# Optimization experiments

Hardware: AMD Instinct MI355X
Metric: run time of the kernel (lower is better)

The kernel has to match this reference:

```python
import math
import jax, jax.numpy as jnp
import numpy as np

B, N, C, H = 8, 512, 1024, 16
HD = C // H


def setup_inputs() -> dict:
    key = jax.random.key(0)
    ks = jax.random.split(key, 10)
    s = 0.02
    return {
        "x": jax.random.normal(ks[0], (B, N, C), jnp.float32),
        "mu": jax.random.normal(ks[1], (B, N, C), jnp.float32),
        "logvar": jax.random.normal(ks[2], (B, N, C), jnp.float32) * 0.1,
        "alpha": jax.random.uniform(ks[3], (B, N, 1), jnp.float32, 0.05, 1.0),
        "pi": jax.random.uniform(ks[4], (B, N, 1), jnp.float32, 0.05, 1.0),
        "z": jax.random.normal(ks[5], (B, N, C), jnp.float32),
        "w_q": jax.random.normal(ks[6], (C, C), jnp.float32) * s,
        "w_k": jax.random.normal(ks[7], (C, C), jnp.float32) * s,
        "w_v": jax.random.normal(ks[8], (C, C), jnp.float32) * s,
        "w_p": jax.random.normal(ks[9], (C, C), jnp.float32) * s,
        "b_p": jnp.zeros((C,), jnp.float32),
    }


def reference(x, mu, logvar, alpha, pi, z, w_q, w_k, w_v, w_p, b_p):
    # Non-meta NVIB path (set_mata_training_mode=False, qkv_bias=False).
    sqrt_hd = math.sqrt(HD)
    q = x @ w_q.T                                   # (B,N,C)
    biased_var = jnp.exp(logvar) + sqrt_hd          # (B,Nl,C)
    k = (mu / biased_var) @ w_k.T                   # (B,Nl,C)
    v = (sqrt_hd / biased_var * mu) @ w_v.T         # (B,Nl,C)

    def split_heads(t):
        b, n, _ = t.shape
        return t.reshape(b, n, H, HD).transpose(0, 2, 1, 3)  # (B,H,n,HD)

    qh, kh, vh = split_heads(q), split_heads(k), split_heads(v)
    attn = jnp.einsum("bhnd,bhmd->bhnm", qh, kh)    # (B,H,N,Nl)
    # additive log-alpha minus L2-norm bias, broadcast over heads and queries
    l2 = 0.5 * jnp.sum((mu / jnp.sqrt(biased_var)) ** 2, axis=-1)  # (B,Nl)
    bias = jnp.log(alpha[..., 0]) - l2              # (B,Nl)
    attn = attn + bias[:, None, None, :]
    attn = jax.nn.softmax(attn, axis=-1)
    out = jnp.einsum("bhnm,bhmd->bhnd", attn, vh)   # (B,H,N,HD)
    out = out.transpose(0, 2, 1, 3).reshape(x.shape[0], x.shape[1], C)
    out = out @ w_p.T + b_p
    return (out, attn)
```

## Files before the change

kernel.cpp:

```cpp
#include <hip/hip_runtime.h>
#include <hip/hip_bf16.h>

#define B_  8
#define N_  512
#define C_  1024
#define H_  16
#define HD_ 64
#define M_  4096

typedef float  f32x4  __attribute__((ext_vector_type(4)));
typedef __bf16 bf16x8 __attribute__((ext_vector_type(8)));
typedef unsigned short ushort_t;

__device__ __forceinline__ ushort_t f2bf(float f) {
  union { float f; unsigned int u; } un; un.f = f;
  unsigned int u = un.u;
  return (ushort_t)((u + 0x7fffu + ((u >> 16) & 1u)) >> 16);
}

__device__ __forceinline__ void gload16(const void* g, void* l) {
  __builtin_amdgcn_global_load_lds((const __attribute__((address_space(1))) void*)g,
                                   (__attribute__((address_space(3))) void*)l, 16, 0, 0);
}
#define SBAR()  __builtin_amdgcn_s_barrier()
#define SCHED() __builtin_amdgcn_sched_barrier(0)
#define VMCNT4() asm volatile("s_waitcnt vmcnt(4)" ::: "memory")
#define VMCNT0() asm volatile("s_waitcnt vmcnt(0)" ::: "memory")


__global__ __launch_bounds__(256) void prep_pack_kernel(
    const float* __restrict__ x, const float* __restrict__ mu,
    const float* __restrict__ logvar,
    const float* __restrict__ wq, const float* __restrict__ wk,
    const float* __restrict__ wv, const float* __restrict__ wp,
    ushort_t* __restrict__ xb, ushort_t* __restrict__ kp, ushort_t* __restrict__ vp,
    ushort_t* __restrict__ wb, float* __restrict__ l2part) {
  const int bid = blockIdx.x, t = threadIdx.x;
  const int row = t >> 1, cg = (t & 1) * 16;
  const int c0 = cg >> 3;

  if (bid < 1024) {
    const int mt = bid >> 5, kt = bid & 31;
    const size_t src = (size_t)(mt * 128 + row) * 1024 + kt * 32 + cg;
    ushort_t tx[16] __attribute__((aligned(16)));
    ushort_t tk[16] __attribute__((aligned(16)));
    ushort_t tv[16] __attribute__((aligned(16)));
    float l2 = 0.f;
#pragma unroll
    for (int j = 0; j < 4; ++j) {
      float4 xv = *(const float4*)(x + src + j * 4);
      float4 mv = *(const float4*)(mu + src + j * 4);
      float4 lv = *(const float4*)(logvar + src + j * 4);
      float xa[4] = {xv.x, xv.y, xv.z, xv.w};
      float ma[4] = {mv.x, mv.y, mv.z, mv.w};
      float la[4] = {lv.x, lv.y, lv.z, lv.w};
#pragma unroll
      for (int i = 0; i < 4; ++i) {
        int e = j * 4 + i;
        float bv  = __expf(la[i]) + 8.0f;
        float inv = 1.0f / bv;
        float kf  = ma[i] * inv;
        l2 += ma[i] * kf;
        tx[e] = f2bf(xa[i]); tk[e] = f2bf(kf); tv[e] = f2bf(8.0f * kf);
      }
    }
    const size_t tb = (size_t)((mt * 32 + kt) * 4) * 1024 + row * 8;
    *(bf16x8*)(xb + tb + c0 * 1024)       = *(const bf16x8*)(tx);
    *(bf16x8*)(xb + tb + (c0 + 1) * 1024) = *(const bf16x8*)(tx + 8);
    *(bf16x8*)(kp + tb + c0 * 1024)       = *(const bf16x8*)(tk);
    *(bf16x8*)(kp + tb + (c0 + 1) * 1024) = *(const bf16x8*)(tk + 8);
    *(bf16x8*)(vp + tb + c0 * 1024)       = *(const bf16x8*)(tv);
    *(bf16x8*)(vp + tb + (c0 + 1) * 1024) = *(const bf16x8*)(tv + 8);
    l2 += __shfl_xor(l2, 1);
    if ((t & 1) == 0) l2part[(size_t)(mt * 128 + row) * 32 + kt] = l2;
  } else {
    const int idx = bid - 1024;
    const int sel = idx >> 8, nt = (idx >> 5) & 7, kt = idx & 31;
    const float* src = sel == 0 ? wq : sel == 1 ? wk : sel == 2 ? wv : wp;
    const size_t so = (size_t)(nt * 128 + row) * 1024 + kt * 32 + cg;
    ushort_t tw[16] __attribute__((aligned(16)));
#pragma unroll
    for (int j = 0; j < 4; ++j) {
      float4 v = *(const float4*)(src + so + j * 4);
      tw[j * 4 + 0] = f2bf(v.x); tw[j * 4 + 1] = f2bf(v.y);
      tw[j * 4 + 2] = f2bf(v.z); tw[j * 4 + 3] = f2bf(v.w);
    }
    ushort_t* dst = wb + (size_t)sel * 1048576;
    const size_t tb = (size_t)((nt * 32 + kt) * 4) * 1024 + row * 8;
    *(bf16x8*)(dst + tb + c0 * 1024)       = *(const bf16x8*)(tw);
    *(bf16x8*)(dst + tb + (c0 + 1) * 1024) = *(const bf16x8*)(tw + 8);
  }
}

__device__ __forceinline__ void gemm_tile_r3(const ushort_t* __restrict__ Ag,
                                             const ushort_t* __restrict__ Wg,
                                             int amt, int ant, f32x4 acc[4][4],
                                             ushort_t* lds) {
  const int t = threadIdx.x;
  const int w = t >> 6, lane = t & 63;
  const int wm = w >> 1, wn = w & 1;
  const int chunk = lane >> 4, r15 = lane & 15;
  const int s0 = t, s1 = t + 256;

#define RSTAGE(kt, buf)                                                           \
  do {                                                                            \
    const ushort_t* sa = Ag + (size_t)(amt * 32 + (kt)) * 4096;                   \
    const ushort_t* sb = Wg + (size_t)(ant * 32 + (kt)) * 4096;                   \
    gload16(sa + s0 * 8, lds + (buf) * 4096 + (s0 & ~63) * 8);                    \
    gload16(sa + s1 * 8, lds + (buf) * 4096 + (s1 & ~63) * 8);                    \
    gload16(sb + s0 * 8, lds + 12288 + (buf) * 4096 + (s0 & ~63) * 8);            \
    gload16(sb + s1 * 8, lds + 12288 + (buf) * 4096 + (s1 & ~63) * 8);            \
  } while (0)

#define RCOMPUTE(j)                                                               \
  do {                                                                            \
    const ushort_t* Ab = lds + (j) * 4096;                                        \
    const ushort_t* Bb = lds + 12288 + (j) * 4096;                                \
    bf16x8 af[4], bw[4];                                                          \
    _Pragma("unroll")                                                             \
    for (int mi = 0; mi < 4; ++mi)                                                \
      af[mi] = *(const bf16x8*)(Ab + (chunk * 128 + wm * 64 + mi * 16 + r15) * 8);\
    _Pragma("unroll")                                                             \
    for (int ni = 0; ni < 4; ++ni)                                                \
      bw[ni] = *(const bf16x8*)(Bb + (chunk * 128 + wn * 64 + ni * 16 + r15) * 8);\
    __builtin_amdgcn_s_setprio(1);                                                \
    _Pragma("unroll")                                                             \
    for (int mi = 0; mi < 4; ++mi)                                                \
      _Pragma("unroll")                                                           \
      for (int ni = 0; ni < 4; ++ni)                                              \
        acc[mi][ni] = __builtin_amdgcn_mfma_f32_16x16x32_bf16(af[mi], bw[ni],     \
                                                              acc[mi][ni], 0, 0, 0); \
    __builtin_amdgcn_s_setprio(0);                                                \
    SCHED();                                                                      \
  } while (0)

  RSTAGE(0, 0); RSTAGE(1, 1);
  VMCNT4();
  SBAR(); SCHED();
  for (int kt0 = 0; kt0 < 30; kt0 += 3) {
    RSTAGE(kt0 + 2, 2); RCOMPUTE(0); VMCNT4(); SBAR(); SCHED();
    RSTAGE(kt0 + 3, 0); RCOMPUTE(1); VMCNT4(); SBAR(); SCHED();
    RSTAGE(kt0 + 4, 1); RCOMPUTE(2); VMCNT4(); SBAR(); SCHED();
  }
  RCOMPUTE(0); VMCNT0(); SBAR(); SCHED();
  RCOMPUTE(1);
#undef RSTAGE
#undef RCOMPUTE
}

__global__ __launch_bounds__(256, 3) void gemm_qkv_kernel(
    const ushort_t* __restrict__ xb, const ushort_t* __restrict__ kp,
    const ushort_t* __restrict__ vp, const ushort_t* __restrict__ wb,
    const float* __restrict__ alpha, const float* __restrict__ l2part,
    float* __restrict__ biasv,
    ushort_t* __restrict__ Qhs, ushort_t* __restrict__ Khs, ushort_t* __restrict__ Vts) {
  __shared__ ushort_t lds[24576];
  const int fid = blockIdx.x;
  const int xcd = fid & 7, vl = fid >> 3;
  const int z = vl >> 5, r = vl & 31;
  const int bx = (xcd & 3) * 8 + (r & 7);
  const int by = (xcd >> 2) * 4 + (r >> 3);
  const ushort_t* Ag = z == 0 ? xb : z == 1 ? kp : vp;
  const ushort_t* Wg = wb + (size_t)z * 1048576;
  const int m0 = bx * 128, n0 = by * 128;
  const int t = threadIdx.x;

  if (z == 0 && by == 0 && t < 128) {
    int row = m0 + t;
    const float* p = l2part + (size_t)row * 32;
    float s = 0.f;
#pragma unroll
    for (int j = 0; j < 8; ++j) {
      float4 v = *(const float4*)(p + j * 4);
      s += (v.x + v.y) + (v.z + v.w);
    }
    biasv[row] = __logf(alpha[row]) - 0.5f * s;
  }

  f32x4 acc[4][4] = {};
  gemm_tile_r3(Ag, Wg, bx, by, acc, lds);
  const int w = t >> 6, lane = t & 63;
  const int wm = w >> 1, wn = w & 1;
  const int hi = lane >> 4, r15 = lane & 15;
  const int b = m0 >> 9, h0 = n0 >> 6;

  __syncthreads();
  if (z < 2) {
    ushort_t* T = lds;
#pragma unroll
    for (int mi = 0; mi < 4; ++mi)
#pragma unroll
      for (int ni = 0; ni < 4; ++ni)
#pragma unroll
        for (int q = 0; q < 4; ++q) {
          int row = wm * 64 + mi * 16 + hi * 4 + q;
          int col = wn * 64 + ni * 16 + r15;
          T[row * 136 + col] = f2bf(acc[mi][ni][q]);
        }
    __syncthreads();
    if (z == 0) {
      const int qt0 = (m0 & 511) >> 6;
#pragma unroll
      for (int i = 0; i < 8; ++i) {
        int c = t + 256 * i;
        int row64 = c & 63, qt_l = (c >> 6) & 1, chunk = (c >> 7) & 7, head_l = (c >> 10) & 1;
        bf16x8 v = *(const bf16x8*)(T + (qt_l * 64 + row64) * 136 + head_l * 64 + chunk * 8);
        int bh = b * 16 + h0 + head_l;
        *(bf16x8*)(Qhs + ((size_t)((bh * 8 + qt0 + qt_l) * 8 + chunk) * 64 + row64) * 8) = v;
      }
    } else {
      const int kt = (m0 & 511) >> 7;
#pragma unroll
      for (int i = 0; i < 8; ++i) {
        int c = t + 256 * i;
        int row128 = c & 127, chunk = (c >> 7) & 7, head_l = (c >> 10) & 1;
        bf16x8 v = *(const bf16x8*)(T + row128 * 136 + head_l * 64 + chunk * 8);
        int bh = b * 16 + h0 + head_l;
        *(bf16x8*)(Khs + ((size_t)((bh * 4 + kt) * 8 + chunk) * 128 + row128) * 8) = v;
      }
    }
  } else {
    ushort_t* T = lds;
#pragma unroll
    for (int mi = 0; mi < 4; ++mi)
#pragma unroll
      for (int ni = 0; ni < 4; ++ni)
#pragma unroll
        for (int q = 0; q < 4; ++q) {
          int row = wm * 64 + mi * 16 + hi * 4 + q;
          int col = wn * 64 + ni * 16 + r15;
          T[row * 129 + col] = f2bf(acc[mi][ni][q]);
        }
    __syncthreads();
    const int kt = (m0 & 511) >> 7;
#pragma unroll
    for (int i = 0; i < 8; ++i) {
      int c = t + 256 * i;
      int d64 = c & 63, head_l = (c >> 6) & 1, chunkp = (c >> 7) & 15;
      bf16x8 v;
#pragma unroll
      for (int j = 0; j < 8; ++j)
        v[j] = *(const __bf16*)(T + (chunkp * 8 + j) * 129 + head_l * 64 + d64);
      int bh = b * 16 + h0 + head_l;
      *(bf16x8*)(Vts + ((size_t)((bh * 4 + kt) * 16 + chunkp) * 64 + d64) * 8) = v;
    }
  }
}

__global__ __launch_bounds__(256, 2) void attn_kernel(
    const ushort_t* __restrict__ Qhs, const ushort_t* __restrict__ Khs,
    const ushort_t* __restrict__ Vts, const float* __restrict__ biasv,
    float* __restrict__ attn_out, ushort_t* __restrict__ Og) {
  __shared__ ushort_t Qt[4096];
  __shared__ ushort_t KV[16384];
  __shared__ ushort_t Pl[8704];
  __shared__ float biasl[512];
  const int fid = blockIdx.x;
  const int v_ = (fid & 7) * 128 + (fid >> 3);
  const int bh = v_ >> 3, qt = v_ & 7;
  const int b = bh >> 4, h = bh & 15;
  const int t = threadIdx.x, w = t >> 6, lane = t & 63;
  const int hi = lane >> 4, r15 = lane & 15;

  {
    float2 bv2 = *(const float2*)(biasv + b * 512 + t * 2);
    biasl[t * 2] = bv2.x; biasl[t * 2 + 1] = bv2.y;
  }
  {
    const ushort_t* sq = Qhs + (size_t)(bh * 8 + qt) * 4096;
    gload16(sq + t * 8, Qt + (t & ~63) * 8);
    gload16(sq + (t + 256) * 8, Qt + ((t + 256) & ~63) * 8);
  }

#define STAGE_K(kt, buf)                                                               \
  do {                                                                                 \
    const ushort_t* sk = Khs + (size_t)(bh * 4 + (kt)) * 8192;                         \
    _Pragma("unroll")                                                                  \
    for (int r = 0; r < 4; ++r) {                                                      \
      int s = r * 256 + t;                                                             \
      gload16(sk + s * 8, KV + (buf) * 8192 + (s & ~63) * 8);                          \
    }                                                                                  \
  } while (0)
#define STAGE_V(kt, buf)                                                               \
  do {                                                                                 \
    const ushort_t* sv = Vts + (size_t)(bh * 4 + (kt)) * 8192;                         \
    _Pragma("unroll")                                                                  \
    for (int r = 0; r < 4; ++r) {                                                      \
      int s = r * 256 + t;                                                             \
      gload16(sv + s * 8, KV + (buf) * 8192 + (s & ~63) * 8);                          \
    }                                                                                  \
  } while (0)

  STAGE_K(0, 0);
  f32x4 acc[32] = {};
  bf16x8 aq[2];
  int cur = 0;

#pragma unroll
  for (int kt = 0; kt < 4; ++kt) {
    if (kt < 3) STAGE_K(kt + 1, cur ^ 1);
    else        STAGE_V(0, cur ^ 1);
    VMCNT4();
    SBAR();
    SCHED();
    if (kt == 0) {
#pragma unroll
      for (int ks = 0; ks < 2; ++ks)
        aq[ks] = *(const bf16x8*)(Qt + ((ks * 4 + hi) * 64 + w * 16 + r15) * 8);
    }
    __builtin_amdgcn_s_setprio(1);
#pragma unroll
    for (int mf = 0; mf < 8; ++mf)
#pragma unroll
      for (int ks = 0; ks < 2; ++ks) {
        bf16x8 bk = *(const bf16x8*)(KV + cur * 8192 + ((ks * 4 + hi) * 128 + mf * 16 + r15) * 8);
        acc[kt * 8 + mf] = __builtin_amdgcn_mfma_f32_16x16x32_bf16(bk, aq[ks], acc[kt * 8 + mf], 0, 0, 0);
      }
    __builtin_amdgcn_s_setprio(0);
    SCHED();
    SBAR();
    SCHED();
    cur ^= 1;
  }

  float mx = -1e30f;
#pragma unroll
  for (int f = 0; f < 32; ++f) {
    f32x4 bv4 = *(const f32x4*)(biasl + f * 16 + hi * 4);
    acc[f] += bv4;
    float m01 = fmaxf(acc[f][0], acc[f][1]);
    float m23 = fmaxf(acc[f][2], acc[f][3]);
    mx = fmaxf(mx, fmaxf(m01, m23));
  }
  mx = fmaxf(mx, __shfl_xor(mx, 16));
  mx = fmaxf(mx, __shfl_xor(mx, 32));
  float sm = 0.f;
#pragma unroll
  for (int f = 0; f < 32; ++f)
#pragma unroll
    for (int q = 0; q < 4; ++q) {
      float p = __expf(acc[f][q] - mx);
      acc[f][q] = p;
      sm += p;
    }
  sm += __shfl_xor(sm, 16);
  sm += __shfl_xor(sm, 32);
  float inv = 1.0f / sm;
#pragma unroll
  for (int f = 0; f < 32; ++f)
#pragma unroll
    for (int q = 0; q < 4; ++q)
      acc[f][q] *= inv;

  ushort_t* Plw = Pl + w * 2176;
  f32x4 oacc[4] = {};
#pragma unroll
  for (int kt = 0; kt < 4; ++kt) {
    if (kt < 3) STAGE_V(kt + 1, cur ^ 1);
#pragma unroll
    for (int fl = 0; fl < 8; ++fl) {
      int f = kt * 8 + fl;
      ushort4 o;
      o.x = f2bf(acc[f][0]); o.y = f2bf(acc[f][1]);
      o.z = f2bf(acc[f][2]); o.w = f2bf(acc[f][3]);
      *(ushort4*)(Plw + r15 * 136 + fl * 16 + hi * 4) = o;
    }
    if (kt < 3) VMCNT4(); else VMCNT0();
    SBAR();
    SCHED();
    __builtin_amdgcn_s_setprio(1);
#pragma unroll
    for (int ks = 0; ks < 4; ++ks) {
      bf16x8 pa = *(const bf16x8*)(Plw + r15 * 136 + ks * 32 + hi * 8);
#pragma unroll
      for (int df = 0; df < 4; ++df) {
        bf16x8 vb = *(const bf16x8*)(KV + cur * 8192 + ((ks * 4 + hi) * 64 + df * 16 + r15) * 8);
        oacc[df] = __builtin_amdgcn_mfma_f32_16x16x32_bf16(pa, vb, oacc[df], 0, 0, 0);
      }
    }
    __builtin_amdgcn_s_setprio(0);
    SCHED();
    SBAR();
    SCHED();
    cur ^= 1;
  }

  {
    float* ao = attn_out + ((size_t)bh * 512 + qt * 64 + w * 16 + r15) * 512 + hi * 4;
#pragma unroll
    for (int f = 0; f < 32; ++f)
      *(f32x4*)(ao + f * 16) = acc[f];
  }

  {
    const int mtile = b * 4 + (qt >> 1);
    const int rowl = (qt & 1) * 64 + w * 16 + hi * 4;
#pragma unroll
    for (int df = 0; df < 4; ++df) {
      int kto = h * 2 + (df >> 1);
      int chunko = (df & 1) * 2 + (r15 >> 3);
      size_t ob = ((size_t)((mtile * 32 + kto) * 4 + chunko) * 1024 + (r15 & 7));
#pragma unroll
      for (int q = 0; q < 4; ++q)
        Og[ob + (size_t)(rowl + q) * 8] = f2bf(oacc[df][q]);
    }
  }
#undef STAGE_K
#undef STAGE_V
}

__global__ __launch_bounds__(256, 3) void gemm_out_kernel(
    const ushort_t* __restrict__ Og, const ushort_t* __restrict__ wb,
    const float* __restrict__ bp, float* __restrict__ out) {
  __shared__ ushort_t lds[24576];
  const int fid = blockIdx.x;
  const int xcd = fid & 7, r = fid >> 3;
  const int bx = (xcd & 3) * 8 + (r & 7);
  const int by = (xcd >> 2) * 4 + (r >> 3);
  const int m0 = bx * 128, n0 = by * 128;
  f32x4 acc[4][4] = {};
  gemm_tile_r3(Og, wb + 3 * 1048576, bx, by, acc, lds);
  const int t = threadIdx.x, w = t >> 6, lane = t & 63;
  const int wm = w >> 1, wn = w & 1;
  const int hi = lane >> 4, r15 = lane & 15;
  float* T2 = (float*)lds;
#pragma unroll
  for (int hh = 0; hh < 2; ++hh) {
    __syncthreads();
    if (wm == hh) {
#pragma unroll
      for (int mi = 0; mi < 4; ++mi)
#pragma unroll
        for (int ni = 0; ni < 4; ++ni)
#pragma unroll
          for (int q = 0; q < 4; ++q) {
            int row = mi * 16 + hi * 4 + q;
            int col = wn * 64 + ni * 16 + r15;
            T2[row * 128 + col] = acc[mi][ni][q];
          }
    }
    __syncthreads();
#pragma unroll
    for (int i = 0; i < 8; ++i) {
      int c = t + 256 * i;
      int row = c >> 5, col0 = (c & 31) * 4;
      float4 v = *(const float4*)(T2 + row * 128 + col0);
      float4 bb = *(const float4*)(bp + n0 + col0);
      v.x += bb.x; v.y += bb.y; v.z += bb.z; v.w += bb.w;
      *(float4*)(out + (size_t)(m0 + hh * 64 + row) * 1024 + n0 + col0) = v;
    }
  }
}

extern "C" void kernel_launch(void* const* d_in, const int* in_sizes, int n_in,
                              void* d_out, int out_size, void* d_ws, size_t ws_size,
                              hipStream_t stream) {
  const float* x      = (const float*)d_in[0];
  const float* mu     = (const float*)d_in[1];
  const float* logvar = (const float*)d_in[2];
  const float* alpha  = (const float*)d_in[3];
  const float* wq = (const float*)d_in[6];
  const float* wk = (const float*)d_in[7];
  const float* wv = (const float*)d_in[8];
  const float* wp = (const float*)d_in[9];
  const float* bp = (const float*)d_in[10];

  float* out      = (float*)d_out;
  float* attn_out = out + (size_t)M_ * C_;

  char* ws = (char*)d_ws;
  ushort_t* xb     = (ushort_t*)(ws);
  ushort_t* kp     = (ushort_t*)(ws + (size_t)8  * 1048576);
  ushort_t* vp     = (ushort_t*)(ws + (size_t)16 * 1048576);
  ushort_t* Qhs    = (ushort_t*)(ws + (size_t)24 * 1048576);
  ushort_t* Khs    = (ushort_t*)(ws + (size_t)32 * 1048576);
  ushort_t* Vts    = (ushort_t*)(ws + (size_t)40 * 1048576);
  ushort_t* wb     = (ushort_t*)(ws + (size_t)48 * 1048576);
  float*    biasv  = (float*)   (ws + (size_t)56 * 1048576);
  float*    l2part = (float*)   (ws + (size_t)57 * 1048576);
  ushort_t* Og     = xb;

  prep_pack_kernel<<<2048, 256, 0, stream>>>(x, mu, logvar, wq, wk, wv, wp,
                                             xb, kp, vp, wb, l2part);
  gemm_qkv_kernel<<<768, 256, 0, stream>>>(xb, kp, vp, wb,
                                           alpha, l2part, biasv,
                                           Qhs, Khs, Vts);
  attn_kernel<<<1024, 256, 0, stream>>>(Qhs, Khs, Vts, biasv, attn_out, Og);
  gemm_out_kernel<<<256, 256, 0, stream>>>(Og, wb, bp, out);
}
```

Before: 110.3 us.

## Load Q, K and V fragments directly from global memory in attention kernel

Removes the LDS staging of Q, K and V tiles, along with the double-buffered async global-to-LDS copies and the block-wide barriers, from the attention kernel. Each wave now reads its MFMA operand fragments straight from global memory, and only the per-wave P tile and the bias stay in shared memory. This cuts LDS usage, which may allow more resident blocks, and drops barrier synchronisation. The cost is that loads are no longer prefetched, so global latency is exposed, and all four waves fetch the same K/V data redundantly through cache.

```diff
diff --git a/kernel.cpp b/kernel.cpp
--- a/kernel.cpp
+++ b/kernel.cpp
@@ -26,6 +26,7 @@
 #define SCHED() __builtin_amdgcn_sched_barrier(0)
 #define VMCNT4() asm volatile("s_waitcnt vmcnt(4)" ::: "memory")
 #define VMCNT0() asm volatile("s_waitcnt vmcnt(0)" ::: "memory")
+#define LGKM0()  asm volatile("s_waitcnt lgkmcnt(0)" ::: "memory")
 
 
 __global__ __launch_bounds__(256) void prep_pack_kernel(
@@ -251,8 +252,6 @@
     const ushort_t* __restrict__ Qhs, const ushort_t* __restrict__ Khs,
     const ushort_t* __restrict__ Vts, const float* __restrict__ biasv,
     float* __restrict__ attn_out, ushort_t* __restrict__ Og) {
-  __shared__ ushort_t Qt[4096];
-  __shared__ ushort_t KV[16384];
   __shared__ ushort_t Pl[8704];
   __shared__ float biasl[512];
   const int fid = blockIdx.x;
@@ -266,61 +265,28 @@
     float2 bv2 = *(const float2*)(biasv + b * 512 + t * 2);
     biasl[t * 2] = bv2.x; biasl[t * 2 + 1] = bv2.y;
   }
-  {
-    const ushort_t* sq = Qhs + (size_t)(bh * 8 + qt) * 4096;
-    gload16(sq + t * 8, Qt + (t & ~63) * 8);
-    gload16(sq + (t + 256) * 8, Qt + ((t + 256) & ~63) * 8);
-  }
-
-#define STAGE_K(kt, buf)                                                               \
-  do {                                                                                 \
-    const ushort_t* sk = Khs + (size_t)(bh * 4 + (kt)) * 8192;                         \
-    _Pragma("unroll")                                                                  \
-    for (int r = 0; r < 4; ++r) {                                                      \
-      int s = r * 256 + t;                                                             \
-      gload16(sk + s * 8, KV + (buf) * 8192 + (s & ~63) * 8);                          \
-    }                                                                                  \
-  } while (0)
-#define STAGE_V(kt, buf)                                                               \
-  do {                                                                                 \
-    const ushort_t* sv = Vts + (size_t)(bh * 4 + (kt)) * 8192;                         \
-    _Pragma("unroll")                                                                  \
-    for (int r = 0; r < 4; ++r) {                                                      \
-      int s = r * 256 + t;                                                             \
-      gload16(sv + s * 8, KV + (buf) * 8192 + (s & ~63) * 8);                          \
-    }                                                                                  \
-  } while (0)
-
-  STAGE_K(0, 0);
+  __syncthreads();
+
+  const ushort_t* sq = Qhs + (size_t)(bh * 8 + qt) * 4096;
+  bf16x8 aq[2];
+#pragma unroll
+  for (int ks = 0; ks < 2; ++ks)
+    aq[ks] = *(const bf16x8*)(sq + ((ks * 4 + hi) * 64 + w * 16 + r15) * 8);
+
+  const ushort_t* Kb = Khs + (size_t)bh * 4 * 8192;
   f32x4 acc[32] = {};
-  bf16x8 aq[2];
-  int cur = 0;
-
 #pragma unroll
   for (int kt = 0; kt < 4; ++kt) {
-    if (kt < 3) STAGE_K(kt + 1, cur ^ 1);
-    else        STAGE_V(0, cur ^ 1);
-    VMCNT4();
-    SBAR();
-    SCHED();
-    if (kt == 0) {
-#pragma unroll
-      for (int ks = 0; ks < 2; ++ks)
-        aq[ks] = *(const bf16x8*)(Qt + ((ks * 4 + hi) * 64 + w * 16 + r15) * 8);
-    }
+    const ushort_t* sk = Kb + kt * 8192;
     __builtin_amdgcn_s_setprio(1);
 #pragma unroll
     for (int mf = 0; mf < 8; ++mf)
 #pragma unroll
       for (int ks = 0; ks < 2; ++ks) {
-        bf16x8 bk = *(const bf16x8*)(KV + cur * 8192 + ((ks * 4 + hi) * 128 + mf * 16 + r15) * 8);
+        bf16x8 bk = *(const bf16x8*)(sk + ((ks * 4 + hi) * 128 + mf * 16 + r15) * 8);
         acc[kt * 8 + mf] = __builtin_amdgcn_mfma_f32_16x16x32_bf16(bk, aq[ks], acc[kt * 8 + mf], 0, 0, 0);
       }
     __builtin_amdgcn_s_setprio(0);
-    SCHED();
-    SBAR();
-    SCHED();
-    cur ^= 1;
   }
 
   float mx = -1e30f;
@@ -353,10 +319,11 @@
       acc[f][q] *= inv;
 
   ushort_t* Plw = Pl + w * 2176;
+  const ushort_t* Vb = Vts + (size_t)bh * 4 * 8192;
   f32x4 oacc[4] = {};
 #pragma unroll
   for (int kt = 0; kt < 4; ++kt) {
-    if (kt < 3) STAGE_V(kt + 1, cur ^ 1);
+    LGKM0(); SCHED();
 #pragma unroll
     for (int fl = 0; fl < 8; ++fl) {
       int f = kt * 8 + fl;
@@ -365,24 +332,19 @@
       o.z = f2bf(acc[f][2]); o.w = f2bf(acc[f][3]);
       *(ushort4*)(Plw + r15 * 136 + fl * 16 + hi * 4) = o;
     }
-    if (kt < 3) VMCNT4(); else VMCNT0();
-    SBAR();
-    SCHED();
+    LGKM0(); SCHED();
+    const ushort_t* sv = Vb + kt * 8192;
     __builtin_amdgcn_s_setprio(1);
 #pragma unroll
     for (int ks = 0; ks < 4; ++ks) {
       bf16x8 pa = *(const bf16x8*)(Plw + r15 * 136 + ks * 32 + hi * 8);
 #pragma unroll
       for (int df = 0; df < 4; ++df) {
-        bf16x8 vb = *(const bf16x8*)(KV + cur * 8192 + ((ks * 4 + hi) * 64 + df * 16 + r15) * 8);
+        bf16x8 vb = *(const bf16x8*)(sv + ((ks * 4 + hi) * 64 + df * 16 + r15) * 8);
         oacc[df] = __builtin_amdgcn_mfma_f32_16x16x32_bf16(pa, vb, oacc[df], 0, 0, 0);
       }
     }
     __builtin_amdgcn_s_setprio(0);
-    SCHED();
-    SBAR();
-    SCHED();
-    cur ^= 1;
   }
 
   {
@@ -405,8 +367,6 @@
         Og[ob + (size_t)(rowl + q) * 8] = f2bf(oacc[df][q]);
     }
   }
-#undef STAGE_K
-#undef STAGE_V
 }
 
 __global__ __launch_bounds__(256, 3) void gemm_out_kernel(
```

After: 126.4 us. 14.5% more time.
